# Kernel tuning notes

Hardware: AMD Instinct MI355X
Metric: run time of the kernel (lower is better)

## Reference

```python
import jax, jax.numpy as jnp
import numpy as np

DX = 0.1  # grid spacing (init arg dx); dy == dx
NX = 4096
NY = 4096


def _pad_bc(X, left, right, top, bottom):
    # X: [1, 1, Nx, Ny]; pad last axis with left/right values, then second-to-last with top/bottom.
    B, C, Nx, Ny = X.shape
    l = jnp.broadcast_to(left, (B, C, Nx, 1)).astype(X.dtype)
    r = jnp.broadcast_to(right, (B, C, Nx, 1)).astype(X.dtype)
    X = jnp.concatenate([l, X, r], axis=3)
    t = jnp.broadcast_to(top, (B, C, 1, Ny + 2)).astype(X.dtype)
    bo = jnp.broadcast_to(bottom, (B, C, 1, Ny + 2)).astype(X.dtype)
    return jnp.concatenate([t, X, bo], axis=2)


def _laplacian(Xp):
    # 5-point stencil, equivalent to conv2d with [[0,1,0],[1,-4,1],[0,1,0]]/dx^2 (valid padding).
    inv_dx2 = 1.0 / (DX * DX)
    return (
        Xp[:, :, :-2, 1:-1]
        + Xp[:, :, 2:, 1:-1]
        + Xp[:, :, 1:-1, :-2]
        + Xp[:, :, 1:-1, 2:]
        - 4.0 * Xp[:, :, 1:-1, 1:-1]
    ) * inv_dx2


def setup_inputs() -> dict:
    key = jax.random.key(0)
    k1, k2 = jax.random.split(key)
    state = jax.random.normal(k1, (1, 2, NX, NY), dtype=jnp.float32)
    bc = jax.random.uniform(k2, (1, 2, 4), dtype=jnp.float32)
    a_org = jnp.asarray(-2.0, dtype=jnp.float32)
    b_org = jnp.asarray(-2.0, dtype=jnp.float32)
    k_org = jnp.asarray(-2.0, dtype=jnp.float32)
    return {"state": state, "bc": bc, "a_org": a_org, "b_org": b_org, "k_org": k_org}


def reference(state, bc, a_org, b_org, k_org):
    a = jax.nn.sigmoid(a_org) * 0.01
    b = jax.nn.sigmoid(b_org) * 0.01
    k = jax.nn.sigmoid(k_org) * 0.01

    U = state[:, :1]  # [1,1,Nx,Ny]
    V = state[:, 1:]

    U_ = _pad_bc(U, bc[0, 0, 0], bc[0, 0, 1], bc[0, 0, 2], bc[0, 0, 3])
    V_ = _pad_bc(V, bc[0, 1, 0], bc[0, 1, 1], bc[0, 1, 2], bc[0, 1, 3])

    delta_u = _laplacian(U_)
    delta_v = _laplacian(V_)

    dUdt = a * delta_u + U - U ** 3 - V - k
    dVdt = b * delta_v + U - V
    return jnp.concatenate([dUdt, dVdt], axis=1)
```

## Files before the change

### kernel.cpp

```cpp
#include <hip/hip_runtime.h>

#define NXD 4096
#define NYD 4096
#define ROWS 4

typedef float f32x4 __attribute__((ext_vector_type(4)));

__global__ __launch_bounds__(256) void DiffReactParamPDE_85478439125433_kernel(
    const float* __restrict__ state,
    const float* __restrict__ bc,
    const float* __restrict__ a_org,
    const float* __restrict__ b_org,
    const float* __restrict__ k_org,
    float* __restrict__ out)
{
    const float inv_dx2 = 100.0f;

    const float a = 0.01f / (1.0f + expf(-a_org[0]));
    const float b = 0.01f / (1.0f + expf(-b_org[0]));
    const float k = 0.01f / (1.0f + expf(-k_org[0]));

    const float uL = bc[0], uR = bc[1], uT = bc[2], uB = bc[3];
    const float vL = bc[4], vR = bc[5], vT = bc[6], vB = bc[7];

    const int j0 = (blockIdx.x * 256 + threadIdx.x) * 4;
    const int i0 = blockIdx.y * ROWS;

    const float* __restrict__ U = state;
    const float* __restrict__ V = state + (size_t)NXD * NYD;
    float* __restrict__ dU = out;
    float* __restrict__ dV = out + (size_t)NXD * NYD;

    const size_t rowbase = (size_t)i0 * NYD + j0;

    float4 u[ROWS + 2], v[ROWS + 2];
#pragma unroll
    for (int r = 0; r < ROWS + 2; ++r) {
        const int row = i0 - 1 + r;
        if (row >= 0 && row < NXD) {
            const size_t bofs = (size_t)row * NYD + j0;
            u[r] = *(const float4*)(U + bofs);
            v[r] = *(const float4*)(V + bofs);
        } else if (row < 0) {
            u[r] = make_float4(uT, uT, uT, uT);
            v[r] = make_float4(vT, vT, vT, vT);
        } else {
            u[r] = make_float4(uB, uB, uB, uB);
            v[r] = make_float4(vB, vB, vB, vB);
        }
    }

    float ulft[ROWS], urgt[ROWS], vlft[ROWS], vrgt[ROWS];
#pragma unroll
    for (int r = 0; r < ROWS; ++r) {
        const size_t bo = rowbase + (size_t)r * NYD;
        ulft[r] = (j0 > 0)       ? U[bo - 1] : uL;
        urgt[r] = (j0 + 4 < NYD) ? U[bo + 4] : uR;
        vlft[r] = (j0 > 0)       ? V[bo - 1] : vL;
        vrgt[r] = (j0 + 4 < NYD) ? V[bo + 4] : vR;
    }

#pragma unroll
    for (int r = 0; r < ROWS; ++r) {
        const float4 cu = u[r + 1], cv = v[r + 1];
        const float4 au = u[r],     bu = u[r + 2];
        const float4 av = v[r],     bv = v[r + 2];

        const float lu0 = (au.x + bu.x + ulft[r] + cu.y - 4.0f * cu.x) * inv_dx2;
        const float lu1 = (au.y + bu.y + cu.x    + cu.z - 4.0f * cu.y) * inv_dx2;
        const float lu2 = (au.z + bu.z + cu.y    + cu.w - 4.0f * cu.z) * inv_dx2;
        const float lu3 = (au.w + bu.w + cu.z + urgt[r] - 4.0f * cu.w) * inv_dx2;

        const float lv0 = (av.x + bv.x + vlft[r] + cv.y - 4.0f * cv.x) * inv_dx2;
        const float lv1 = (av.y + bv.y + cv.x    + cv.z - 4.0f * cv.y) * inv_dx2;
        const float lv2 = (av.z + bv.z + cv.y    + cv.w - 4.0f * cv.z) * inv_dx2;
        const float lv3 = (av.w + bv.w + cv.z + vrgt[r] - 4.0f * cv.w) * inv_dx2;

        f32x4 duo, dvo;
        duo.x = a * lu0 + cu.x - cu.x * cu.x * cu.x - cv.x - k;
        duo.y = a * lu1 + cu.y - cu.y * cu.y * cu.y - cv.y - k;
        duo.z = a * lu2 + cu.z - cu.z * cu.z * cu.z - cv.z - k;
        duo.w = a * lu3 + cu.w - cu.w * cu.w * cu.w - cv.w - k;

        dvo.x = b * lv0 + cu.x - cv.x;
        dvo.y = b * lv1 + cu.y - cv.y;
        dvo.z = b * lv2 + cu.z - cv.z;
        dvo.w = b * lv3 + cu.w - cv.w;

        const size_t bo = rowbase + (size_t)r * NYD;
        __builtin_nontemporal_store(duo, (f32x4*)(dU + bo));
        __builtin_nontemporal_store(dvo, (f32x4*)(dV + bo));
    }
}

extern "C" void kernel_launch(void* const* d_in, const int* in_sizes, int n_in,
                              void* d_out, int out_size, void* d_ws, size_t ws_size,
                              hipStream_t stream) {
    const float* state = (const float*)d_in[0];
    const float* bc    = (const float*)d_in[1];
    const float* a_org = (const float*)d_in[2];
    const float* b_org = (const float*)d_in[3];
    const float* k_org = (const float*)d_in[4];
    float* out = (float*)d_out;

    dim3 block(256, 1, 1);
    dim3 grid(NYD / (4 * 256), NXD / ROWS, 1);
    DiffReactParamPDE_85478439125433_kernel<<<grid, block, 0, stream>>>(
        state, bc, a_org, b_org, k_org, out);
}
```

Before: 250.3 us.

## Use rolling row registers, wavefront shuffles for horizontal halo, and taller row tiles

Each thread now processes 8 rows per block instead of 4 and keeps a rolling three-row register window, prefetching the next row inside the loop. Horizontal neighbours come from wavefront shuffles, so only the edge lanes of each 64-lane wave issue scalar halo loads, replacing per-thread unaligned scalar loads for every row. This cuts redundant halo traffic and halves the vertical-halo overhead, but it leaves fewer blocks in the grid and adds shuffle instructions plus lane-dependent branches.

```diff
diff --git a/kernel.cpp b/kernel.cpp
--- a/kernel.cpp
+++ b/kernel.cpp
@@ -2,7 +2,7 @@
 
 #define NXD 4096
 #define NYD 4096
-#define ROWS 4
+#define ROWS 8
 
 typedef float f32x4 __attribute__((ext_vector_type(4)));
 
@@ -23,6 +23,7 @@
     const float uL = bc[0], uR = bc[1], uT = bc[2], uB = bc[3];
     const float vL = bc[4], vR = bc[5], vT = bc[6], vB = bc[7];
 
+    const int lane = threadIdx.x & 63;
     const int j0 = (blockIdx.x * 256 + threadIdx.x) * 4;
     const int i0 = blockIdx.y * ROWS;
 
@@ -31,66 +32,82 @@
     float* __restrict__ dU = out;
     float* __restrict__ dV = out + (size_t)NXD * NYD;
 
-    const size_t rowbase = (size_t)i0 * NYD + j0;
+    const float4 fuT = make_float4(uT, uT, uT, uT), fuB = make_float4(uB, uB, uB, uB);
+    const float4 fvT = make_float4(vT, vT, vT, vT), fvB = make_float4(vB, vB, vB, vB);
 
-    float4 u[ROWS + 2], v[ROWS + 2];
-#pragma unroll
-    for (int r = 0; r < ROWS + 2; ++r) {
-        const int row = i0 - 1 + r;
-        if (row >= 0 && row < NXD) {
-            const size_t bofs = (size_t)row * NYD + j0;
-            u[r] = *(const float4*)(U + bofs);
-            v[r] = *(const float4*)(V + bofs);
-        } else if (row < 0) {
-            u[r] = make_float4(uT, uT, uT, uT);
-            v[r] = make_float4(vT, vT, vT, vT);
-        } else {
-            u[r] = make_float4(uB, uB, uB, uB);
-            v[r] = make_float4(vB, vB, vB, vB);
-        }
+#define LD4(P, ROW) (*(const float4*)((P) + (size_t)(ROW) * NYD + j0))
+
+    float4 um, uc, up, vm, vc, vp;
+    if (i0 > 0) { um = LD4(U, i0 - 1); vm = LD4(V, i0 - 1); }
+    else        { um = fuT;            vm = fvT; }
+    uc = LD4(U, i0); vc = LD4(V, i0);
+    if (i0 + 1 < NXD) { up = LD4(U, i0 + 1); vp = LD4(V, i0 + 1); }
+    else              { up = fuB;            vp = fvB; }
+
+    float eLu = uL, eRu = uR, eLv = vL, eRv = vR;
+    if (lane == 0 && j0 > 0) {
+        eLu = U[(size_t)i0 * NYD + j0 - 1];
+        eLv = V[(size_t)i0 * NYD + j0 - 1];
     }
-
-    float ulft[ROWS], urgt[ROWS], vlft[ROWS], vrgt[ROWS];
-#pragma unroll
-    for (int r = 0; r < ROWS; ++r) {
-        const size_t bo = rowbase + (size_t)r * NYD;
-        ulft[r] = (j0 > 0)       ? U[bo - 1] : uL;
-        urgt[r] = (j0 + 4 < NYD) ? U[bo + 4] : uR;
-        vlft[r] = (j0 > 0)       ? V[bo - 1] : vL;
-        vrgt[r] = (j0 + 4 < NYD) ? V[bo + 4] : vR;
+    if (lane == 63 && j0 + 4 < NYD) {
+        eRu = U[(size_t)i0 * NYD + j0 + 4];
+        eRv = V[(size_t)i0 * NYD + j0 + 4];
     }
 
 #pragma unroll
     for (int r = 0; r < ROWS; ++r) {
-        const float4 cu = u[r + 1], cv = v[r + 1];
-        const float4 au = u[r],     bu = u[r + 2];
-        const float4 av = v[r],     bv = v[r + 2];
+        const int row = i0 + r;
 
-        const float lu0 = (au.x + bu.x + ulft[r] + cu.y - 4.0f * cu.x) * inv_dx2;
-        const float lu1 = (au.y + bu.y + cu.x    + cu.z - 4.0f * cu.y) * inv_dx2;
-        const float lu2 = (au.z + bu.z + cu.y    + cu.w - 4.0f * cu.z) * inv_dx2;
-        const float lu3 = (au.w + bu.w + cu.z + urgt[r] - 4.0f * cu.w) * inv_dx2;
+        float4 un = fuB, vn = fvB;
+        float eLu_n = uL, eRu_n = uR, eLv_n = vL, eRv_n = vR;
+        if (r < ROWS - 1) {
+            const int rn = row + 2;
+            if (rn < NXD) { un = LD4(U, rn); vn = LD4(V, rn); }
+            if (lane == 0 && j0 > 0) {
+                eLu_n = U[(size_t)(row + 1) * NYD + j0 - 1];
+                eLv_n = V[(size_t)(row + 1) * NYD + j0 - 1];
+            }
+            if (lane == 63 && j0 + 4 < NYD) {
+                eRu_n = U[(size_t)(row + 1) * NYD + j0 + 4];
+                eRv_n = V[(size_t)(row + 1) * NYD + j0 + 4];
+            }
+        }
 
-        const float lv0 = (av.x + bv.x + vlft[r] + cv.y - 4.0f * cv.x) * inv_dx2;
-        const float lv1 = (av.y + bv.y + cv.x    + cv.z - 4.0f * cv.y) * inv_dx2;
-        const float lv2 = (av.z + bv.z + cv.y    + cv.w - 4.0f * cv.z) * inv_dx2;
-        const float lv3 = (av.w + bv.w + cv.z + vrgt[r] - 4.0f * cv.w) * inv_dx2;
+        float ulft = __shfl_up(uc.w, 1);   if (lane == 0)  ulft = eLu;
+        float urgt = __shfl_down(uc.x, 1); if (lane == 63) urgt = eRu;
+        float vlft = __shfl_up(vc.w, 1);   if (lane == 0)  vlft = eLv;
+        float vrgt = __shfl_down(vc.x, 1); if (lane == 63) vrgt = eRv;
+
+        const float lu0 = (um.x + up.x + ulft + uc.y - 4.0f * uc.x) * inv_dx2;
+        const float lu1 = (um.y + up.y + uc.x + uc.z - 4.0f * uc.y) * inv_dx2;
+        const float lu2 = (um.z + up.z + uc.y + uc.w - 4.0f * uc.z) * inv_dx2;
+        const float lu3 = (um.w + up.w + uc.z + urgt - 4.0f * uc.w) * inv_dx2;
+
+        const float lv0 = (vm.x + vp.x + vlft + vc.y - 4.0f * vc.x) * inv_dx2;
+        const float lv1 = (vm.y + vp.y + vc.x + vc.z - 4.0f * vc.y) * inv_dx2;
+        const float lv2 = (vm.z + vp.z + vc.y + vc.w - 4.0f * vc.z) * inv_dx2;
+        const float lv3 = (vm.w + vp.w + vc.z + vrgt - 4.0f * vc.w) * inv_dx2;
 
         f32x4 duo, dvo;
-        duo.x = a * lu0 + cu.x - cu.x * cu.x * cu.x - cv.x - k;
-        duo.y = a * lu1 + cu.y - cu.y * cu.y * cu.y - cv.y - k;
-        duo.z = a * lu2 + cu.z - cu.z * cu.z * cu.z - cv.z - k;
-        duo.w = a * lu3 + cu.w - cu.w * cu.w * cu.w - cv.w - k;
+        duo.x = a * lu0 + uc.x - uc.x * uc.x * uc.x - vc.x - k;
+        duo.y = a * lu1 + uc.y - uc.y * uc.y * uc.y - vc.y - k;
+        duo.z = a * lu2 + uc.z - uc.z * uc.z * uc.z - vc.z - k;
+        duo.w = a * lu3 + uc.w - uc.w * uc.w * uc.w - vc.w - k;
 
-        dvo.x = b * lv0 + cu.x - cv.x;
-        dvo.y = b * lv1 + cu.y - cv.y;
-        dvo.z = b * lv2 + cu.z - cv.z;
-        dvo.w = b * lv3 + cu.w - cv.w;
+        dvo.x = b * lv0 + uc.x - vc.x;
+        dvo.y = b * lv1 + uc.y - vc.y;
+        dvo.z = b * lv2 + uc.z - vc.z;
+        dvo.w = b * lv3 + uc.w - vc.w;
 
-        const size_t bo = rowbase + (size_t)r * NYD;
+        const size_t bo = (size_t)row * NYD + j0;
         __builtin_nontemporal_store(duo, (f32x4*)(dU + bo));
         __builtin_nontemporal_store(dvo, (f32x4*)(dV + bo));
+
+        um = uc; uc = up; up = un;
+        vm = vc; vc = vp; vp = vn;
+        eLu = eLu_n; eRu = eRu_n; eLv = eLv_n; eRv = eRv_n;
     }
+#undef LD4
 }
 
 extern "C" void kernel_launch(void* const* d_in, const int* in_sizes, int n_in,
```

Measured after the change: 245.2 us. 2.0% less time.
